# Kernel tuning notes

Hardware: AMD Instinct MI355X
Metric: run time of the kernel (lower is better)

## Reference

```python
import jax, jax.numpy as jnp
import numpy as np

COMMA_ID = 1010   # BERT wordpiece id for ','
H, NH, HD = 768, 8, 96
B, S = 64, 512
NSEG = 17         # 16 commas per row -> 17 segments
EPS = 1e-5


def setup_inputs() -> dict:
    key = jax.random.key(0)
    ks = jax.random.split(key, 16)
    text_hs = jax.random.normal(ks[0], (B, S, H), jnp.float32)
    cols_hs = jax.random.normal(ks[1], (B, S, H), jnp.float32)
    ids = jax.random.randint(ks[2], (B, S), 0, 30522)
    ids = jnp.where(ids == COMMA_ID, COMMA_ID + 1, ids)  # avoid accidental commas
    comma_pos = jnp.arange(16, 257, 16)                  # 16 commas per row
    ids = ids.at[:, comma_pos].set(COMMA_ID)
    sc = 0.02
    wq = jax.random.normal(ks[3], (H, H), jnp.float32) * sc
    wk = jax.random.normal(ks[4], (H, H), jnp.float32) * sc
    wv = jax.random.normal(ks[5], (H, H), jnp.float32) * sc
    bq = jnp.zeros((H,), jnp.float32)
    bk = jnp.zeros((H,), jnp.float32)
    bv = jnp.zeros((H,), jnp.float32)
    wo = jax.random.normal(ks[6], (H, H), jnp.float32) * sc
    bo = jnp.zeros((H,), jnp.float32)
    gamma = jnp.ones((H,), jnp.float32)
    beta = jnp.zeros((H,), jnp.float32)
    w_out = jax.random.normal(ks[7], (1, H), jnp.float32) * sc
    b_out = jnp.zeros((1,), jnp.float32)
    return dict(text_hs=text_hs, cols_hs=cols_hs, wq=wq, wk=wk, wv=wv,
                bq=bq, bk=bk, bv=bv, wo=wo, bo=bo, gamma=gamma, beta=beta,
                w_out=w_out, b_out=b_out, columns_input_ids=ids, n_segments=NSEG)


def _forward(text_hs, cols_hs, wq, wk, wv, bq, bk, bv, wo, bo,
             gamma, beta, w_out, b_out, columns_input_ids, n_segments):
    t = text_hs[:, 1:, :]   # drop first token, as in forward()  [B, L, H]
    c = cols_hs[:, 1:, :]
    L = t.shape[1]
    # --- nn.MultiheadAttention(query=cols, key=value=text), batch_first ---
    q = c @ wq.T + bq
    k = t @ wk.T + bk
    v = t @ wv.T + bv
    split = lambda x: x.reshape(x.shape[0], -1, NH, HD).transpose(0, 2, 1, 3)
    scores = jnp.einsum('bhqd,bhkd->bhqk', split(q), split(k)) / np.sqrt(HD).astype(np.float32)
    attn = jax.nn.softmax(scores, axis=-1)
    ctx = jnp.einsum('bhqk,bhkd->bhqd', attn, split(v))
    ctx = ctx.transpose(0, 2, 1, 3).reshape(c.shape[0], L, H)
    attn_out = ctx @ wo.T + bo
    # --- BatchNorm1d over channels (training-mode batch stats) ---
    xt = attn_out.transpose(0, 2, 1)            # [B, H, L]
    mu = xt.mean(axis=(0, 2), keepdims=True)
    var = xt.var(axis=(0, 2), keepdims=True)     # biased, as torch BN normalization
    xn = (xt - mu) / jnp.sqrt(var + EPS) * gamma[None, :, None] + beta[None, :, None]
    cross_out = c + xn.transpose(0, 2, 1)       # residual add
    fv = (cross_out @ w_out.T + b_out).squeeze(-1)   # [B, L] scores per token
    # --- compose_outputs: mean-pool comma-delimited ragged spans ---
    is_comma = columns_input_ids[:, :L] == COMMA_ID
    seg = jnp.cumsum(is_comma.astype(jnp.int32), axis=1) - is_comma.astype(jnp.int32)
    mask = (jnp.arange(L)[None, :] >= 1) & (~is_comma)    # slice_start=1, commas excluded
    oh = ((seg[:, :, None] == jnp.arange(n_segments)[None, None, :])
          & mask[:, :, None]).astype(fv.dtype)            # [B, L, J]
    sums = jnp.einsum('blj,bl->bj', oh, fv)
    cnt = oh.sum(axis=1)
    return sums / jnp.maximum(cnt, 1.0)                   # [B, n_segments]


def reference(text_hs, cols_hs, wq, wk, wv, bq, bk, bv, wo, bo,
              gamma, beta, w_out, b_out, columns_input_ids, n_segments):
    return _forward(text_hs, cols_hs, wq, wk, wv, bq, bk, bv, wo, bo,
                    gamma, beta, w_out, b_out, columns_input_ids, n_segments)
```

## Files before the change

### kernel.cpp

```cpp
#include <hip/hip_runtime.h>
#include <hip/hip_bf16.h>

#define COMMA_IDC 1010
#define NHEAD 8
#define Ll 511
#define Mrows 32704
#define NSEG 17

typedef __attribute__((ext_vector_type(8))) short bf16x8;
typedef __attribute__((ext_vector_type(4))) float f32x4;
typedef unsigned short u16;
typedef unsigned int u32;
typedef unsigned long long u64;

__device__ __forceinline__ u16 f2b(float f) {
  __hip_bfloat16 h = __float2bfloat16(f);
  return *reinterpret_cast<u16*>(&h);
}
__device__ __forceinline__ float b2f(u16 u) {
  u32 x = ((u32)u) << 16;
  return __builtin_bit_cast(float, x);
}

__device__ __forceinline__ void gld_lds16(const void* g, void* l) {
  __builtin_amdgcn_global_load_lds(
      (const __attribute__((address_space(1))) void*)(u64)g,
      (__attribute__((address_space(3))) void*)(u32)(u64)l,
      16, 0, 0);
}

#define MFMA16(a, b, c) __builtin_amdgcn_mfma_f32_16x16x32_bf16(a, b, c, 0, 0, 0)

__global__ void conv_sliced2(const float4* __restrict__ s0, const float4* __restrict__ s1,
                             ushort4* __restrict__ d0, ushort4* __restrict__ d1) {
  const float4* src = blockIdx.z ? s1 : s0;
  ushort4* dst = blockIdx.z ? d1 : d0;
  int b = blockIdx.y;
  int idx = blockIdx.x * 256 + threadIdx.x;
  if (idx >= Ll * 192) return;
  int l = idx / 192, c = idx - l * 192;
  float4 v = src[(b * 512 + l + 1) * 192 + c];
  ushort4 o; o.x = f2b(v.x); o.y = f2b(v.y); o.z = f2b(v.z); o.w = f2b(v.w);
  dst[(b * Ll + l) * 192 + c] = o;
}

__global__ void conv_w(const float4* __restrict__ wq, const float4* __restrict__ wk,
                       const float4* __restrict__ wv, const float4* __restrict__ wo,
                       ushort4* __restrict__ wqkvb, ushort4* __restrict__ wob) {
  int i = blockIdx.x * 256 + threadIdx.x;
  int seg = i / 147456, off = i - seg * 147456;
  const float4* s = (seg == 0) ? wq : ((seg == 1) ? wk : ((seg == 2) ? wv : wo));
  ushort4* d = (seg == 3) ? wob : (wqkvb + seg * 147456);
  float4 v = s[off];
  ushort4 o; o.x = f2b(v.x); o.y = f2b(v.y); o.z = f2b(v.z); o.w = f2b(v.w);
  d[off] = o;
}

__global__ void zero_kernel(float* p, int n) {
  int i = blockIdx.x * 256 + threadIdx.x;
  if (i < n) p[i] = 0.f;
}

#define LDA_(i, kk) (*(const bf16x8*)(sMem + bA + ((i) * 16 + fr) * 64 + ((((kk) * 4 + fq) ^ xm) << 3)))
#define LDW_(j, kk) (*(const bf16x8*)(sMem + bW + (((wc * 64 + (j) * 16) >> 7) * 8192) + \
                     (((wc * 64 + (j) * 16) & 127) + fr) * 64 + ((((kk) * 4 + fq) ^ xm) << 3)))
#define LGKM0 do { asm volatile("s_waitcnt lgkmcnt(0)" ::: "memory"); __builtin_amdgcn_sched_barrier(0); } while (0)

template<int NTILES, int NOUT, int QNT>
__global__ __launch_bounds__(512, 2) void gemm256(
    const u16* __restrict__ A0, const u16* __restrict__ A1, const u16* __restrict__ W,
    const float* __restrict__ b0, const float* __restrict__ b1, const float* __restrict__ b2,
    u16* __restrict__ outp)
{
  __shared__ __align__(16) u16 sMem[65536];
  const int tid = threadIdx.x;
  const int lane = tid & 63, wid = tid >> 6;
  const int fr = lane & 15, fq = lane >> 4;
  const int wr = wid >> 2, wc = wid & 3;
  const int xm = fr & 7;

  int fid = blockIdx.x;
  int xcd = fid & 7, w = fid >> 3;
  int mrow = xcd * 16 + w / NTILES;
  int ncol = w - (w / NTILES) * NTILES;
  const int m0 = mrow * 256, n0 = ncol * 256;
  const u16* __restrict__ A = (ncol < QNT) ? A0 : A1;

  const int rS = tid >> 3;
  const int cS = (tid & 7) ^ (rS & 7);
  const u16* gA0 = A + (u64)(m0 + rS) * 768 + cS * 8;
  const u16* gA1 = A + (u64)(m0 + 128 + rS) * 768 + cS * 8;
  const u16* gW0 = W + (u64)(n0 + rS) * 768 + cS * 8;
  const u16* gW1 = W + (u64)(n0 + 128 + rS) * 768 + cS * 8;
  const u32 st0 = tid * 8;

  f32x4 acc[8][4] = {};

  auto stage_all = [&](int buf, int kt) {
    const int kb = kt * 64;
    const u32 db = (u32)buf * 32768;
    gld_lds16(gA0 + kb, sMem + db + st0);
    gld_lds16(gA0 + kb + 49152, sMem + db + st0 + 4096);
    gld_lds16(gA1 + kb, sMem + db + 8192 + st0);
    gld_lds16(gA1 + kb + 49152, sMem + db + 8192 + st0 + 4096);
    gld_lds16(gW0 + kb, sMem + db + 16384 + st0);
    gld_lds16(gW0 + kb + 49152, sMem + db + 16384 + st0 + 4096);
    gld_lds16(gW1 + kb, sMem + db + 24576 + st0);
    gld_lds16(gW1 + kb + 49152, sMem + db + 24576 + st0 + 4096);
  };

  stage_all(0, 0);
  asm volatile("s_waitcnt vmcnt(0)" ::: "memory");
  __builtin_amdgcn_s_barrier();

  for (int kt = 0; kt < 12; ++kt) {
    const u32 db = (u32)(kt & 1) * 32768;
    const u32 bA = db + wr * 8192;
    const u32 bW = db + 16384;
    bf16x8 af[4][2], wf[2][2];

#pragma unroll
    for (int i = 0; i < 4; i++) { af[i][0] = LDA_(i, 0); af[i][1] = LDA_(i, 1); }
#pragma unroll
    for (int j = 0; j < 2; j++) { wf[j][0] = LDW_(j, 0); wf[j][1] = LDW_(j, 1); }
    __builtin_amdgcn_s_barrier();
    if (kt + 1 < 12) stage_all((kt + 1) & 1, kt + 1);
    LGKM0;
    __builtin_amdgcn_s_setprio(1);
#pragma unroll
    for (int i = 0; i < 4; i++)
#pragma unroll
      for (int j = 0; j < 2; j++) {
        acc[i][j] = MFMA16(af[i][0], wf[j][0], acc[i][j]);
        acc[i][j] = MFMA16(af[i][1], wf[j][1], acc[i][j]);
      }
    __builtin_amdgcn_s_setprio(0);
    __builtin_amdgcn_s_barrier();

#pragma unroll
    for (int j = 0; j < 2; j++) { wf[j][0] = LDW_(j + 2, 0); wf[j][1] = LDW_(j + 2, 1); }
    __builtin_amdgcn_s_barrier();
    LGKM0;
    __builtin_amdgcn_s_setprio(1);
#pragma unroll
    for (int i = 0; i < 4; i++)
#pragma unroll
      for (int j = 0; j < 2; j++) {
        acc[i][j + 2] = MFMA16(af[i][0], wf[j][0], acc[i][j + 2]);
        acc[i][j + 2] = MFMA16(af[i][1], wf[j][1], acc[i][j + 2]);
      }
    __builtin_amdgcn_s_setprio(0);
    __builtin_amdgcn_s_barrier();

#pragma unroll
    for (int i = 0; i < 4; i++) { af[i][0] = LDA_(i + 4, 0); af[i][1] = LDA_(i + 4, 1); }
#pragma unroll
    for (int j = 0; j < 2; j++) { wf[j][0] = LDW_(j, 0); wf[j][1] = LDW_(j, 1); }
    __builtin_amdgcn_s_barrier();
    LGKM0;
    __builtin_amdgcn_s_setprio(1);
#pragma unroll
    for (int i = 0; i < 4; i++)
#pragma unroll
      for (int j = 0; j < 2; j++) {
        acc[i + 4][j] = MFMA16(af[i][0], wf[j][0], acc[i + 4][j]);
        acc[i + 4][j] = MFMA16(af[i][1], wf[j][1], acc[i + 4][j]);
      }
    __builtin_amdgcn_s_setprio(0);
    __builtin_amdgcn_s_barrier();

#pragma unroll
    for (int j = 0; j < 2; j++) { wf[j][0] = LDW_(j + 2, 0); wf[j][1] = LDW_(j + 2, 1); }
    __builtin_amdgcn_s_barrier();
    LGKM0;
    __builtin_amdgcn_s_setprio(1);
#pragma unroll
    for (int i = 0; i < 4; i++)
#pragma unroll
      for (int j = 0; j < 2; j++) {
        acc[i + 4][j + 2] = MFMA16(af[i][0], wf[j][0], acc[i + 4][j + 2]);
        acc[i + 4][j + 2] = MFMA16(af[i][1], wf[j][1], acc[i + 4][j + 2]);
      }
    __builtin_amdgcn_s_setprio(0);
    asm volatile("s_waitcnt vmcnt(0)" ::: "memory");
    __builtin_amdgcn_s_barrier();
  }

  const float* bp = (n0 < 768) ? b0 : ((n0 < 1536) ? b1 : b2);
  const int bcol = n0 & 767;
  float bj[4];
#pragma unroll
  for (int j = 0; j < 4; j++) bj[j] = bp[bcol + wc * 64 + j * 16 + fr];

#pragma unroll
  for (int h = 0; h < 2; h++) {
    __syncthreads();
    if (wr == h) {
#pragma unroll
      for (int i = 0; i < 8; i++)
#pragma unroll
        for (int j = 0; j < 4; j++)
#pragma unroll
          for (int r = 0; r < 4; r++)
            sMem[(i * 16 + fq * 4 + r) * 264 + wc * 64 + j * 16 + fr] = f2b(acc[i][j][r] + bj[j]);
    }
    __syncthreads();
#pragma unroll
    for (int it = 0; it < 8; it++) {
      int chunk = tid + it * 512;
      int lr = chunk >> 5, ch = chunk & 31;
      *(bf16x8*)(outp + (u64)(m0 + h * 128 + lr) * NOUT + n0 + ch * 8) =
          *(const bf16x8*)(sMem + lr * 264 + ch * 8);
    }
  }
}

__global__ __launch_bounds__(256) void vtrans(const u16* __restrict__ QKV, u16* __restrict__ VT) {
  __shared__ __align__(16) u16 sT[128 * 128];
  int bh = blockIdx.y;
  int b = bh >> 3, h = bh & 7;
  int l0 = blockIdx.x * 128;
  u16* outp = VT + (u64)bh * 96 * 512;
  int t = threadIdx.x;
#pragma unroll
  for (int k = 0; k < 6; k++) {
    int c = t + k * 256;
    int l = c / 12, ch = c - l * 12;
    int lc = l0 + l; if (lc > 510) lc = 510;
    bf16x8 v = *(const bf16x8*)(QKV + (u64)(b * 511 + lc) * 2304 + 1536 + h * 96 + ch * 8);
    int chunk = l * 16 + (ch ^ ((l >> 3) & 7));
    *(bf16x8*)(sT + chunk * 8) = v;
  }
  __syncthreads();
#pragma unroll
  for (int k = 0; k < 6; k++) {
    int c = t + k * 256;
    int d = c >> 4, lch = c & 15;
    u16 vals[8];
#pragma unroll
    for (int k2 = 0; k2 < 8; k2++) {
      int r = lch * 8 + k2;
      int idx = r * 128 + (((d >> 3) ^ (lch & 7)) << 3) + (d & 7);
      vals[k2] = sT[idx];
    }
    bf16x8 o;
#pragma unroll
    for (int k2 = 0; k2 < 8; k2++) o[k2] = (short)vals[k2];
    *(bf16x8*)(outp + (u64)d * 512 + l0 + lch * 8) = o;
  }
}

#define PST 36
__global__ __launch_bounds__(256) void attn_kernel(
    const u16* __restrict__ QKV, const u16* __restrict__ VT, u16* __restrict__ ctxb)
{
  __shared__ __align__(16) u16 sK[32 * 96];
  __shared__ __align__(16) u16 sV[32 * 96];
  __shared__ __align__(16) u16 sP[4][16 * PST];
  const int tid = threadIdx.x, lane = tid & 63, wid = tid >> 6;
  int fid = blockIdx.x;
  int xcd = fid & 7, slot = (fid >> 3) & 3, grp = fid >> 5;
  int bh = grp * 8 + xcd;
  int b = bh >> 3, h = bh & 7;
  int q0 = slot * 128;
  const int fr = lane & 15, fq = lane >> 4;
  const u64 mb = (u64)(b * 511);
  const u64 hbV = (u64)bh * 96 * 512;

  bf16x8 qf[2][3];
#pragma unroll
  for (int sub = 0; sub < 2; sub++) {
    int qr = q0 + wid * 32 + sub * 16 + fr; if (qr > 510) qr = 510;
#pragma unroll
    for (int ks = 0; ks < 3; ks++)
      qf[sub][ks] = *(const bf16x8*)(QKV + (mb + qr) * 2304 + h * 96 + ks * 32 + fq * 8);
  }

  f32x4 ctx[2][6] = {};
  f32x4 sumP[2] = {};

  int cK1 = wid * 64 + lane;
  int kr1 = cK1 / 12, kc1 = cK1 - kr1 * 12;
  const u16* gK1 = QKV + (mb + kr1) * 2304 + 768 + h * 96 + kc1 * 8;
  int cK2 = 256 + cK1;
  int kr2 = cK2 / 12, kc2 = cK2 - kr2 * 12;
  const u16* gK2 = QKV + (mb + kr2) * 2304 + 768 + h * 96 + kc2 * 8;
  int cV1 = wid * 64 + lane;
  int dV1 = cV1 >> 2, jV1 = (cV1 & 3) ^ ((dV1 >> 1) & 3);
  const u16* gV1 = VT + hbV + (u64)dV1 * 512 + jV1 * 8;
  int cV2 = 256 + (wid - 2) * 64 + lane;
  int dV2 = cV2 >> 2, jV2 = (cV2 & 3) ^ ((dV2 >> 1) & 3);
  const u16* gV2 = VT + hbV + (u64)dV2 * 512 + jV2 * 8;

  u16* lK1 = sK + (u32)(wid * 64) * 8;
  u16* lK2 = sK + (u32)(256 + wid * 64) * 8;
  u16* lV1 = sV + (u32)(wid * 64) * 8;
  u16* lV2 = sV + (u32)(256 + (wid - 2) * 64) * 8;
  u16* pw = &sP[wid][0];

  const float cs = 0.10206207261596575f;
  const int cpx = fq ^ ((fr >> 1) & 3);

  for (int kv0 = 0; kv0 < 511; kv0 += 32) {
    __syncthreads();
    gld_lds16(gK1, lK1); gK1 += (u64)32 * 2304;
    if (wid < 2) { gld_lds16(gK2, lK2); gK2 += (u64)32 * 2304; }
    gld_lds16(gV1, lV1); gV1 += 32;
    if (wid >= 2) { gld_lds16(gV2, lV2); gV2 += 32; }
    __syncthreads();

    bf16x8 kf0[3], kf1[3];
#pragma unroll
    for (int ks = 0; ks < 3; ks++) {
      kf0[ks] = *(const bf16x8*)(sK + fr * 96 + ks * 32 + fq * 8);
      kf1[ks] = *(const bf16x8*)(sK + (16 + fr) * 96 + ks * 32 + fq * 8);
    }
    const bool ok1 = (kv0 + 16 + fr) < Ll;

#pragma unroll
    for (int sub = 0; sub < 2; sub++) {
      f32x4 s0 = {}, s1 = {};
#pragma unroll
      for (int ks = 0; ks < 3; ks++) {
        s0 = MFMA16(qf[sub][ks], kf0[ks], s0);
        s1 = MFMA16(qf[sub][ks], kf1[ks], s1);
      }
      float p0[4], p1[4];
#pragma unroll
      for (int r = 0; r < 4; r++) {
        p0[r] = __expf(s0[r] * cs);
        float e1 = __expf(s1[r] * cs);
        p1[r] = ok1 ? e1 : 0.f;
        sumP[sub][r] += p0[r] + p1[r];
      }
#pragma unroll
      for (int r = 0; r < 4; r++) {
        int row = fq * 4 + r;
        pw[row * PST + fr] = f2b(p0[r]);
        pw[row * PST + 16 + fr] = f2b(p1[r]);
      }
      bf16x8 pf = *(const bf16x8*)(pw + fr * PST + fq * 8);
#pragma unroll
      for (int df = 0; df < 6; df++) {
        bf16x8 vf = *(const bf16x8*)(sV + (df * 16 + fr) * 32 + cpx * 8);
        ctx[sub][df] = MFMA16(pf, vf, ctx[sub][df]);
      }
    }
  }

#pragma unroll
  for (int sub = 0; sub < 2; sub++) {
    float inv[4];
#pragma unroll
    for (int r = 0; r < 4; r++) {
      float s = sumP[sub][r];
      s += __shfl_xor(s, 1, 64);
      s += __shfl_xor(s, 2, 64);
      s += __shfl_xor(s, 4, 64);
      s += __shfl_xor(s, 8, 64);
      inv[r] = 1.f / s;
    }
#pragma unroll
    for (int df = 0; df < 6; df++) {
#pragma unroll
      for (int r = 0; r < 4; r++) {
        int q = q0 + wid * 32 + sub * 16 + fq * 4 + r;
        if (q < Ll)
          ctxb[(u64)(b * Ll + q) * 768 + h * 96 + df * 16 + fr] = f2b(ctx[sub][df][r] * inv[r]);
      }
    }
  }
}

__global__ __launch_bounds__(256) void stats_kernel(const u16* __restrict__ ao,
                                                    float* __restrict__ ssum, float* __restrict__ ssq)
{
  int t = threadIdx.x;
  int row0 = blockIdx.x * 128;
  int rowEnd = row0 + 128; if (rowEnd > Mrows) rowEnd = Mrows;
  float s[3] = {0.f, 0.f, 0.f}, q[3] = {0.f, 0.f, 0.f};
  for (int m = row0; m < rowEnd; m++) {
    const u16* rp = ao + (u64)m * 768;
#pragma unroll
    for (int i = 0; i < 3; i++) {
      float v = b2f(rp[t + i * 256]);
      s[i] += v; q[i] += v * v;
    }
  }
#pragma unroll
  for (int i = 0; i < 3; i++) {
    atomicAdd(&ssum[t + i * 256], s[i]);
    atomicAdd(&ssq[t + i * 256], q[i]);
  }
}

__global__ __launch_bounds__(256) void derived_kernel(
    const float* __restrict__ ssum, const float* __restrict__ ssq,
    const float* __restrict__ w_out, const float* __restrict__ b_out,
    const float* __restrict__ gamma, const float* __restrict__ beta,
    float* __restrict__ weff, float* __restrict__ consts)
{
  __shared__ float red[256];
  int t = threadIdx.x;
  float acc = 0.f;
  const float invN = 1.f / 32704.f;
#pragma unroll
  for (int i = 0; i < 3; i++) {
    int hh = t + i * 256;
    float mu = ssum[hh] * invN;
    float var = ssq[hh] * invN - mu * mu;
    float rstd = 1.f / sqrtf(var + 1e-5f);
    float we = w_out[hh] * gamma[hh] * rstd;
    weff[hh] = we;
    acc += w_out[hh] * beta[hh] - we * mu;
  }
  red[t] = acc; __syncthreads();
  for (int s = 128; s > 0; s >>= 1) { if (t < s) red[t] += red[t + s]; __syncthreads(); }
  if (t == 0) consts[0] = b_out[0] + red[0];
}

__global__ __launch_bounds__(256) void fv_kernel(
    const u16* __restrict__ ao, const u16* __restrict__ cb,
    const float* __restrict__ w_out, const float* __restrict__ weff,
    const float* __restrict__ consts, float* __restrict__ fv)
{
  int lane = threadIdx.x & 63, wid = threadIdx.x >> 6;
  int m = blockIdx.x * 4 + wid;
  if (m >= Mrows) return;
  const u16* ap = ao + (u64)m * 768;
  const u16* cp = cb + (u64)m * 768;
  float acc = 0.f;
#pragma unroll
  for (int i = 0; i < 12; i++) {
    int hh = lane + i * 64;
    acc += b2f(ap[hh]) * weff[hh] + b2f(cp[hh]) * w_out[hh];
  }
#pragma unroll
  for (int off = 1; off < 64; off <<= 1) acc += __shfl_xor(acc, off, 64);
  if (lane == 0) fv[m] = acc + consts[0];
}

__global__ __launch_bounds__(64) void seg_kernel(
    const float* __restrict__ fv, const int* __restrict__ ids, float* __restrict__ out)
{
  __shared__ float ssum[NSEG];
  __shared__ int scnt[NSEG];
  int lane = threadIdx.x;
  int b = blockIdx.x;
  if (lane < NSEG) { ssum[lane] = 0.f; scnt[lane] = 0; }
  __syncthreads();
  int carry = 0;
  for (int it = 0; it < 8; it++) {
    int l = it * 64 + lane;
    bool active = l < Ll;
    int id = active ? ids[b * 512 + l] : 0;
    bool comma = active && (id == COMMA_IDC);
    u64 cmask = __ballot(comma);
    int seg = carry + __popcll(cmask & ((1ull << lane) - 1ull));
    bool valid = active && (l >= 1) && !comma;
    if (valid && seg < NSEG) {
      atomicAdd(&ssum[seg], fv[b * Ll + l]);
      atomicAdd(&scnt[seg], 1);
    }
    carry += __popcll(cmask);
  }
  __syncthreads();
  if (lane < NSEG) {
    float c = (float)scnt[lane];
    out[b * NSEG + lane] = ssum[lane] / fmaxf(c, 1.f);
  }
}

extern "C" void kernel_launch(void* const* d_in, const int* in_sizes, int n_in,
                              void* d_out, int out_size, void* d_ws, size_t ws_size,
                              hipStream_t stream)
{
  const float* text  = (const float*)d_in[0];
  const float* cols  = (const float*)d_in[1];
  const float* wq    = (const float*)d_in[2];
  const float* wk    = (const float*)d_in[3];
  const float* wvp   = (const float*)d_in[4];
  const float* bq    = (const float*)d_in[5];
  const float* bk    = (const float*)d_in[6];
  const float* bv    = (const float*)d_in[7];
  const float* wo    = (const float*)d_in[8];
  const float* bo    = (const float*)d_in[9];
  const float* gamma = (const float*)d_in[10];
  const float* beta  = (const float*)d_in[11];
  const float* w_out = (const float*)d_in[12];
  const float* b_out = (const float*)d_in[13];
  const int*   ids   = (const int*)d_in[14];
  float* out = (float*)d_out;

  char* ws = (char*)d_ws;
  u16* cb    = (u16*)(ws + 0ull);
  u16* tb    = (u16*)(ws + 50331648ull);
  u16* wqkvb = (u16*)(ws + 100663296ull);
  u16* wob   = (u16*)(ws + 104202240ull);
  u16* QKVb  = (u16*)(ws + 105381888ull);
  u16* ctxb  = (u16*)(ws + 256376832ull);
  u16* VTb   = tb;
  u16* aob   = QKVb;
  float* ssum   = (float*)(ws + 105381888ull + 50331648ull);
  float* ssq    = ssum + 768;
  float* weff   = ssum + 1536;
  float* consts = ssum + 2304;
  float* fv     = (float*)((char*)ssum + 16384ull);

  conv_sliced2<<<dim3(384, 64, 2), 256, 0, stream>>>(
      (const float4*)cols, (const float4*)text, (ushort4*)cb, (ushort4*)tb);
  conv_w<<<2304, 256, 0, stream>>>(
      (const float4*)wq, (const float4*)wk, (const float4*)wvp, (const float4*)wo,
      (ushort4*)wqkvb, (ushort4*)wob);

  gemm256<9, 2304, 3><<<1152, 512, 0, stream>>>(cb, tb, wqkvb, bq, bk, bv, QKVb);
  vtrans<<<dim3(4, 512), 256, 0, stream>>>(QKVb, VTb);
  attn_kernel<<<2048, 256, 0, stream>>>(QKVb, VTb, ctxb);

  zero_kernel<<<6, 256, 0, stream>>>(ssum, 1536);
  gemm256<3, 768, 99><<<384, 512, 0, stream>>>(ctxb, ctxb, wob, bo, bo, bo, aob);
  stats_kernel<<<256, 256, 0, stream>>>(aob, ssum, ssq);
  derived_kernel<<<1, 256, 0, stream>>>(ssum, ssq, w_out, b_out, gamma, beta, weff, consts);
  fv_kernel<<<8176, 256, 0, stream>>>(aob, cb, w_out, weff, consts, fv);
  seg_kernel<<<64, 64, 0, stream>>>(fv, ids, out);
}
```

Before: 460.2 us.

## Fuse fp32 input conversion into QKV GEMM, BN stats into out-proj, widen attention tile

The separate fp32-to-bf16 slice/convert kernel is removed. The QKV GEMM now loads fp32 activations from the original tensors into registers, converts them, and writes them to LDS, double-buffered with a deeper prefetch. The output-projection GEMM accumulates BatchNorm column sums and sums of squares in its epilogue via atomics, which replaces the stats pass over the output. The attention kernel processes 64 keys per step instead of 32, with new LDS swizzles. The GEMM inner loop is also restructured to load all W fragments at once with fewer barriers, and fv reads the fp32 columns directly. This saves bandwidth and kernel launches, at the cost of register pressure, a different bf16 rounding path for the stats, and a more complex attention tile.

```diff
diff --git a/kernel.cpp b/kernel.cpp
--- a/kernel.cpp
+++ b/kernel.cpp
@@ -30,19 +30,7 @@
 }
 
 #define MFMA16(a, b, c) __builtin_amdgcn_mfma_f32_16x16x32_bf16(a, b, c, 0, 0, 0)
-
-__global__ void conv_sliced2(const float4* __restrict__ s0, const float4* __restrict__ s1,
-                             ushort4* __restrict__ d0, ushort4* __restrict__ d1) {
-  const float4* src = blockIdx.z ? s1 : s0;
-  ushort4* dst = blockIdx.z ? d1 : d0;
-  int b = blockIdx.y;
-  int idx = blockIdx.x * 256 + threadIdx.x;
-  if (idx >= Ll * 192) return;
-  int l = idx / 192, c = idx - l * 192;
-  float4 v = src[(b * 512 + l + 1) * 192 + c];
-  ushort4 o; o.x = f2b(v.x); o.y = f2b(v.y); o.z = f2b(v.z); o.w = f2b(v.w);
-  dst[(b * Ll + l) * 192 + c] = o;
-}
+#define LGKM0 do { asm volatile("s_waitcnt lgkmcnt(0)" ::: "memory"); __builtin_amdgcn_sched_barrier(0); } while (0)
 
 __global__ void conv_w(const float4* __restrict__ wq, const float4* __restrict__ wk,
                        const float4* __restrict__ wv, const float4* __restrict__ wo,
@@ -61,16 +49,15 @@
   if (i < n) p[i] = 0.f;
 }
 
-#define LDA_(i, kk) (*(const bf16x8*)(sMem + bA + ((i) * 16 + fr) * 64 + ((((kk) * 4 + fq) ^ xm) << 3)))
-#define LDW_(j, kk) (*(const bf16x8*)(sMem + bW + (((wc * 64 + (j) * 16) >> 7) * 8192) + \
+#define LDA(db, i, kk) (*(const bf16x8*)(sMem + (db) + wr * 8192 + ((i) * 16 + fr) * 64 + ((((kk) * 4 + fq) ^ xm) << 3)))
+#define LDW(db, j, kk) (*(const bf16x8*)(sMem + (db) + 16384 + (((wc * 64 + (j) * 16) >> 7) * 8192) + \
                      (((wc * 64 + (j) * 16) & 127) + fr) * 64 + ((((kk) * 4 + fq) ^ xm) << 3)))
-#define LGKM0 do { asm volatile("s_waitcnt lgkmcnt(0)" ::: "memory"); __builtin_amdgcn_sched_barrier(0); } while (0)
-
-template<int NTILES, int NOUT, int QNT>
+
+template<int NTILES, int NOUT, int QNT, bool AF32, bool DO_STATS>
 __global__ __launch_bounds__(512, 2) void gemm256(
-    const u16* __restrict__ A0, const u16* __restrict__ A1, const u16* __restrict__ W,
+    const void* __restrict__ A0v, const void* __restrict__ A1v, const u16* __restrict__ W,
     const float* __restrict__ b0, const float* __restrict__ b1, const float* __restrict__ b2,
-    u16* __restrict__ outp)
+    u16* __restrict__ outp, float* __restrict__ ssum, float* __restrict__ ssq)
 {
   __shared__ __align__(16) u16 sMem[65536];
   const int tid = threadIdx.x;
@@ -84,113 +71,167 @@
   int mrow = xcd * 16 + w / NTILES;
   int ncol = w - (w / NTILES) * NTILES;
   const int m0 = mrow * 256, n0 = ncol * 256;
-  const u16* __restrict__ A = (ncol < QNT) ? A0 : A1;
 
   const int rS = tid >> 3;
   const int cS = (tid & 7) ^ (rS & 7);
-  const u16* gA0 = A + (u64)(m0 + rS) * 768 + cS * 8;
-  const u16* gA1 = A + (u64)(m0 + 128 + rS) * 768 + cS * 8;
   const u16* gW0 = W + (u64)(n0 + rS) * 768 + cS * 8;
   const u16* gW1 = W + (u64)(n0 + 128 + rS) * 768 + cS * 8;
   const u32 st0 = tid * 8;
 
+  const float* fA = (ncol < QNT) ? (const float*)A0v : (const float*)A1v;
+  const u16*   uA = (ncol < QNT) ? (const u16*)A0v : (const u16*)A1v;
+  const float* aSrc[4];
+  u32 aDst[4];
+  if constexpr (AF32) {
+#pragma unroll
+    for (int c4 = 0; c4 < 4; c4++) {
+      int c = tid + c4 * 512;
+      int half = c >> 10, rowin = (c >> 3) & 127, p = c & 7;
+      int m = m0 + half * 128 + rowin;
+      if (m > Mrows - 1) m = Mrows - 1;
+      int srcrow = m + m / 511 + 1;
+      int s = p ^ (rowin & 7);
+      aSrc[c4] = fA + (u64)srcrow * 768 + s * 8;
+      aDst[c4] = (u32)(half * 8192 + rowin * 64 + p * 8);
+    }
+  }
+  const u16* gA0u = nullptr;
+  const u16* gA1u = nullptr;
+  if constexpr (!AF32) {
+    gA0u = uA + (u64)(m0 + rS) * 768 + cS * 8;
+    gA1u = uA + (u64)(m0 + 128 + rS) * 768 + cS * 8;
+  }
+
   f32x4 acc[8][4] = {};
-
-  auto stage_all = [&](int buf, int kt) {
+  bf16x8 af[4][2], wf[4][2];
+  float4 rA[8];
+
+  auto stageW = [&](int buf, int kt) {
+    const int kb = kt * 64;
+    const u32 db = (u32)buf * 32768 + 16384;
+    gld_lds16(gW0 + kb, sMem + db + st0);
+    gld_lds16(gW0 + kb + 49152, sMem + db + st0 + 4096);
+    gld_lds16(gW1 + kb, sMem + db + 8192 + st0);
+    gld_lds16(gW1 + kb + 49152, sMem + db + 8192 + st0 + 4096);
+  };
+  auto stageAu = [&](int buf, int kt) {
     const int kb = kt * 64;
     const u32 db = (u32)buf * 32768;
-    gld_lds16(gA0 + kb, sMem + db + st0);
-    gld_lds16(gA0 + kb + 49152, sMem + db + st0 + 4096);
-    gld_lds16(gA1 + kb, sMem + db + 8192 + st0);
-    gld_lds16(gA1 + kb + 49152, sMem + db + 8192 + st0 + 4096);
-    gld_lds16(gW0 + kb, sMem + db + 16384 + st0);
-    gld_lds16(gW0 + kb + 49152, sMem + db + 16384 + st0 + 4096);
-    gld_lds16(gW1 + kb, sMem + db + 24576 + st0);
-    gld_lds16(gW1 + kb + 49152, sMem + db + 24576 + st0 + 4096);
+    gld_lds16(gA0u + kb, sMem + db + st0);
+    gld_lds16(gA0u + kb + 49152, sMem + db + st0 + 4096);
+    gld_lds16(gA1u + kb, sMem + db + 8192 + st0);
+    gld_lds16(gA1u + kb + 49152, sMem + db + 8192 + st0 + 4096);
   };
-
-  stage_all(0, 0);
-  asm volatile("s_waitcnt vmcnt(0)" ::: "memory");
+  auto loadA = [&](int kt) {
+#pragma unroll
+    for (int c4 = 0; c4 < 4; c4++) {
+      rA[2 * c4]     = *(const float4*)(aSrc[c4] + kt * 64);
+      rA[2 * c4 + 1] = *(const float4*)(aSrc[c4] + kt * 64 + 4);
+    }
+  };
+  auto writeA = [&](int buf) {
+    const u32 db = (u32)buf * 32768;
+#pragma unroll
+    for (int c4 = 0; c4 < 4; c4++) {
+      const float4 x = rA[2 * c4], y = rA[2 * c4 + 1];
+      bf16x8 v;
+      v[0] = (short)f2b(x.x); v[1] = (short)f2b(x.y); v[2] = (short)f2b(x.z); v[3] = (short)f2b(x.w);
+      v[4] = (short)f2b(y.x); v[5] = (short)f2b(y.y); v[6] = (short)f2b(y.z); v[7] = (short)f2b(y.w);
+      *(bf16x8*)(sMem + db + aDst[c4]) = v;
+    }
+  };
+
+  if constexpr (AF32) {
+    stageW(0, 0);
+    loadA(0);
+    writeA(0);
+    loadA(1);
+  } else {
+    stageAu(0, 0);
+    stageW(0, 0);
+    asm volatile("s_waitcnt vmcnt(0)" ::: "memory");
+  }
+  LGKM0;
   __builtin_amdgcn_s_barrier();
 
   for (int kt = 0; kt < 12; ++kt) {
     const u32 db = (u32)(kt & 1) * 32768;
-    const u32 bA = db + wr * 8192;
-    const u32 bW = db + 16384;
-    bf16x8 af[4][2], wf[2][2];
-
-#pragma unroll
-    for (int i = 0; i < 4; i++) { af[i][0] = LDA_(i, 0); af[i][1] = LDA_(i, 1); }
-#pragma unroll
-    for (int j = 0; j < 2; j++) { wf[j][0] = LDW_(j, 0); wf[j][1] = LDW_(j, 1); }
-    __builtin_amdgcn_s_barrier();
-    if (kt + 1 < 12) stage_all((kt + 1) & 1, kt + 1);
-    LGKM0;
-    __builtin_amdgcn_s_setprio(1);
-#pragma unroll
-    for (int i = 0; i < 4; i++)
-#pragma unroll
-      for (int j = 0; j < 2; j++) {
-        acc[i][j] = MFMA16(af[i][0], wf[j][0], acc[i][j]);
-        acc[i][j] = MFMA16(af[i][1], wf[j][1], acc[i][j]);
-      }
-    __builtin_amdgcn_s_setprio(0);
-    __builtin_amdgcn_s_barrier();
-
-#pragma unroll
-    for (int j = 0; j < 2; j++) { wf[j][0] = LDW_(j + 2, 0); wf[j][1] = LDW_(j + 2, 1); }
+#pragma unroll
+    for (int i = 0; i < 4; i++) { af[i][0] = LDA(db, i, 0); af[i][1] = LDA(db, i, 1); }
+#pragma unroll
+    for (int j = 0; j < 4; j++) { wf[j][0] = LDW(db, j, 0); wf[j][1] = LDW(db, j, 1); }
+    if (kt + 1 < 12) {
+      if constexpr (AF32) {
+        writeA((kt + 1) & 1);
+        stageW((kt + 1) & 1, kt + 1);
+        if (kt + 2 < 12) loadA(kt + 2);
+      } else {
+        stageAu((kt + 1) & 1, kt + 1);
+        stageW((kt + 1) & 1, kt + 1);
+      }
+    }
     __builtin_amdgcn_s_barrier();
     LGKM0;
     __builtin_amdgcn_s_setprio(1);
 #pragma unroll
     for (int i = 0; i < 4; i++)
 #pragma unroll
-      for (int j = 0; j < 2; j++) {
-        acc[i][j + 2] = MFMA16(af[i][0], wf[j][0], acc[i][j + 2]);
-        acc[i][j + 2] = MFMA16(af[i][1], wf[j][1], acc[i][j + 2]);
+      for (int j = 0; j < 4; j++) {
+        acc[i][j] = MFMA16(af[i][0], wf[j][0], acc[i][j]);
+        acc[i][j] = MFMA16(af[i][1], wf[j][1], acc[i][j]);
       }
     __builtin_amdgcn_s_setprio(0);
     __builtin_amdgcn_s_barrier();
-
-#pragma unroll
-    for (int i = 0; i < 4; i++) { af[i][0] = LDA_(i + 4, 0); af[i][1] = LDA_(i + 4, 1); }
-#pragma unroll
-    for (int j = 0; j < 2; j++) { wf[j][0] = LDW_(j, 0); wf[j][1] = LDW_(j, 1); }
-    __builtin_amdgcn_s_barrier();
+#pragma unroll
+    for (int i = 0; i < 4; i++) { af[i][0] = LDA(db, i + 4, 0); af[i][1] = LDA(db, i + 4, 1); }
     LGKM0;
     __builtin_amdgcn_s_setprio(1);
 #pragma unroll
     for (int i = 0; i < 4; i++)
 #pragma unroll
-      for (int j = 0; j < 2; j++) {
+      for (int j = 0; j < 4; j++) {
         acc[i + 4][j] = MFMA16(af[i][0], wf[j][0], acc[i + 4][j]);
         acc[i + 4][j] = MFMA16(af[i][1], wf[j][1], acc[i + 4][j]);
       }
     __builtin_amdgcn_s_setprio(0);
+    if (kt + 1 < 12) {
+      if constexpr (AF32) {
+        if (kt + 2 < 12) { asm volatile("s_waitcnt vmcnt(8)" ::: "memory"); }
+        else             { asm volatile("s_waitcnt vmcnt(0)" ::: "memory"); }
+      } else {
+        asm volatile("s_waitcnt vmcnt(0)" ::: "memory");
+      }
+    }
     __builtin_amdgcn_s_barrier();
-
-#pragma unroll
-    for (int j = 0; j < 2; j++) { wf[j][0] = LDW_(j + 2, 0); wf[j][1] = LDW_(j + 2, 1); }
-    __builtin_amdgcn_s_barrier();
-    LGKM0;
-    __builtin_amdgcn_s_setprio(1);
-#pragma unroll
-    for (int i = 0; i < 4; i++)
-#pragma unroll
-      for (int j = 0; j < 2; j++) {
-        acc[i + 4][j + 2] = MFMA16(af[i][0], wf[j][0], acc[i + 4][j + 2]);
-        acc[i + 4][j + 2] = MFMA16(af[i][1], wf[j][1], acc[i + 4][j + 2]);
-      }
-    __builtin_amdgcn_s_setprio(0);
-    asm volatile("s_waitcnt vmcnt(0)" ::: "memory");
-    __builtin_amdgcn_s_barrier();
   }
 
   const float* bp = (n0 < 768) ? b0 : ((n0 < 1536) ? b1 : b2);
-  const int bcol = n0 & 767;
+  const int bcol = n0 % 768;
   float bj[4];
 #pragma unroll
   for (int j = 0; j < 4; j++) bj[j] = bp[bcol + wc * 64 + j * 16 + fr];
+
+  if constexpr (DO_STATS) {
+#pragma unroll
+    for (int j = 0; j < 4; j++) {
+      float s = 0.f, q = 0.f;
+#pragma unroll
+      for (int i = 0; i < 8; i++)
+#pragma unroll
+        for (int r = 0; r < 4; r++) {
+          int m = m0 + wr * 128 + i * 16 + fq * 4 + r;
+          float v = acc[i][j][r] + bj[j];
+          if (m < Mrows) { s += v; q += v * v; }
+        }
+      s += __shfl_xor(s, 16, 64); s += __shfl_xor(s, 32, 64);
+      q += __shfl_xor(q, 16, 64); q += __shfl_xor(q, 32, 64);
+      if (fq == 0) {
+        int col = n0 + wc * 64 + j * 16 + fr;
+        atomicAdd(&ssum[col], s);
+        atomicAdd(&ssq[col], q);
+      }
+    }
+  }
 
 #pragma unroll
   for (int h = 0; h < 2; h++) {
@@ -250,12 +291,12 @@
   }
 }
 
-#define PST 36
+#define PST 68
 __global__ __launch_bounds__(256) void attn_kernel(
     const u16* __restrict__ QKV, const u16* __restrict__ VT, u16* __restrict__ ctxb)
 {
-  __shared__ __align__(16) u16 sK[32 * 96];
-  __shared__ __align__(16) u16 sV[32 * 96];
+  __shared__ __align__(16) u16 sK[64 * 96];
+  __shared__ __align__(16) u16 sV[96 * 64];
   __shared__ __align__(16) u16 sP[4][16 * PST];
   const int tid = threadIdx.x, lane = tid & 63, wid = tid >> 6;
   int fid = blockIdx.x;
@@ -279,71 +320,79 @@
   f32x4 ctx[2][6] = {};
   f32x4 sumP[2] = {};
 
-  int cK1 = wid * 64 + lane;
-  int kr1 = cK1 / 12, kc1 = cK1 - kr1 * 12;
-  const u16* gK1 = QKV + (mb + kr1) * 2304 + 768 + h * 96 + kc1 * 8;
-  int cK2 = 256 + cK1;
-  int kr2 = cK2 / 12, kc2 = cK2 - kr2 * 12;
-  const u16* gK2 = QKV + (mb + kr2) * 2304 + 768 + h * 96 + kc2 * 8;
-  int cV1 = wid * 64 + lane;
-  int dV1 = cV1 >> 2, jV1 = (cV1 & 3) ^ ((dV1 >> 1) & 3);
-  const u16* gV1 = VT + hbV + (u64)dV1 * 512 + jV1 * 8;
-  int cV2 = 256 + (wid - 2) * 64 + lane;
-  int dV2 = cV2 >> 2, jV2 = (cV2 & 3) ^ ((dV2 >> 1) & 3);
-  const u16* gV2 = VT + hbV + (u64)dV2 * 512 + jV2 * 8;
-
-  u16* lK1 = sK + (u32)(wid * 64) * 8;
-  u16* lK2 = sK + (u32)(256 + wid * 64) * 8;
-  u16* lV1 = sV + (u32)(wid * 64) * 8;
-  u16* lV2 = sV + (u32)(256 + (wid - 2) * 64) * 8;
+  int kRow[3]; u32 kOffG[3], vOffG[3];
+  u16 *kDst[3], *vDst[3];
+#pragma unroll
+  for (int k = 0; k < 3; k++) {
+    int c = wid * 64 + lane + k * 256;
+    int r = c / 12, p = c - r * 12;
+    int s = p - (r % 12); if (s < 0) s += 12;
+    kRow[k] = r;
+    kOffG[k] = 768 + h * 96 + s * 8;
+    kDst[k] = sK + (u32)(wid * 64 + k * 256) * 8;
+    int d = c >> 3, pv = c & 7;
+    int sv = pv ^ (d & 7);
+    vOffG[k] = (u32)(d * 512 + sv * 8);
+    vDst[k] = sV + (u32)(wid * 64 + k * 256) * 8;
+  }
+
+  const float cs = 0.10206207261596575f;
   u16* pw = &sP[wid][0];
 
-  const float cs = 0.10206207261596575f;
-  const int cpx = fq ^ ((fr >> 1) & 3);
-
-  for (int kv0 = 0; kv0 < 511; kv0 += 32) {
+  for (int kv0 = 0; kv0 < 511; kv0 += 64) {
     __syncthreads();
-    gld_lds16(gK1, lK1); gK1 += (u64)32 * 2304;
-    if (wid < 2) { gld_lds16(gK2, lK2); gK2 += (u64)32 * 2304; }
-    gld_lds16(gV1, lV1); gV1 += 32;
-    if (wid >= 2) { gld_lds16(gV2, lV2); gV2 += 32; }
+#pragma unroll
+    for (int k = 0; k < 3; k++) {
+      int row = kv0 + kRow[k]; if (row > 510) row = 510;
+      gld_lds16(QKV + (mb + row) * 2304 + kOffG[k], kDst[k]);
+    }
+#pragma unroll
+    for (int k = 0; k < 3; k++)
+      gld_lds16(VT + hbV + vOffG[k] + kv0, vDst[k]);
     __syncthreads();
 
-    bf16x8 kf0[3], kf1[3];
-#pragma unroll
-    for (int ks = 0; ks < 3; ks++) {
-      kf0[ks] = *(const bf16x8*)(sK + fr * 96 + ks * 32 + fq * 8);
-      kf1[ks] = *(const bf16x8*)(sK + (16 + fr) * 96 + ks * 32 + fq * 8);
-    }
-    const bool ok1 = (kv0 + 16 + fr) < Ll;
+    bf16x8 kf[4][3];
+#pragma unroll
+    for (int kv16 = 0; kv16 < 4; kv16++) {
+      int r = kv16 * 16 + fr;
+      int rm = r % 12;
+#pragma unroll
+      for (int ks = 0; ks < 3; ks++) {
+        int sidx = ks * 4 + fq + rm; if (sidx >= 12) sidx -= 12;
+        kf[kv16][ks] = *(const bf16x8*)(sK + (r * 12 + sidx) * 8);
+      }
+    }
 
 #pragma unroll
     for (int sub = 0; sub < 2; sub++) {
-      f32x4 s0 = {}, s1 = {};
-#pragma unroll
-      for (int ks = 0; ks < 3; ks++) {
-        s0 = MFMA16(qf[sub][ks], kf0[ks], s0);
-        s1 = MFMA16(qf[sub][ks], kf1[ks], s1);
-      }
-      float p0[4], p1[4];
-#pragma unroll
-      for (int r = 0; r < 4; r++) {
-        p0[r] = __expf(s0[r] * cs);
-        float e1 = __expf(s1[r] * cs);
-        p1[r] = ok1 ? e1 : 0.f;
-        sumP[sub][r] += p0[r] + p1[r];
-      }
-#pragma unroll
-      for (int r = 0; r < 4; r++) {
-        int row = fq * 4 + r;
-        pw[row * PST + fr] = f2b(p0[r]);
-        pw[row * PST + 16 + fr] = f2b(p1[r]);
-      }
-      bf16x8 pf = *(const bf16x8*)(pw + fr * PST + fq * 8);
+      f32x4 s[4] = {};
+#pragma unroll
+      for (int kv16 = 0; kv16 < 4; kv16++)
+#pragma unroll
+        for (int ks = 0; ks < 3; ks++)
+          s[kv16] = MFMA16(qf[sub][ks], kf[kv16][ks], s[kv16]);
+
+#pragma unroll
+      for (int kv16 = 0; kv16 < 4; kv16++) {
+        bool ok = (kv0 + kv16 * 16 + fr) < Ll;
+#pragma unroll
+        for (int r = 0; r < 4; r++) {
+          float e = __expf(s[kv16][r] * cs);
+          e = ok ? e : 0.f;
+          sumP[sub][r] += e;
+          pw[(fq * 4 + r) * PST + kv16 * 16 + fr] = f2b(e);
+        }
+      }
+      bf16x8 pf0 = *(const bf16x8*)(pw + fr * PST + fq * 8);
+      bf16x8 pf1 = *(const bf16x8*)(pw + fr * PST + 32 + fq * 8);
 #pragma unroll
       for (int df = 0; df < 6; df++) {
-        bf16x8 vf = *(const bf16x8*)(sV + (df * 16 + fr) * 32 + cpx * 8);
-        ctx[sub][df] = MFMA16(pf, vf, ctx[sub][df]);
+        int row = df * 16 + fr;
+        int xv = fr & 7;
+        bf16x8 vf0 = *(const bf16x8*)(sV + row * 64 + ((fq ^ xv) << 3));
+        bf16x8 vf1 = *(const bf16x8*)(sV + row * 64 + (((4 + fq) ^ xv) << 3));
+        ctx[sub][df] = MFMA16(pf0, vf0, ctx[sub][df]);
+        ctx[sub][df] = MFMA16(pf1, vf1, ctx[sub][df]);
       }
     }
   }
@@ -369,28 +418,6 @@
           ctxb[(u64)(b * Ll + q) * 768 + h * 96 + df * 16 + fr] = f2b(ctx[sub][df][r] * inv[r]);
       }
     }
-  }
-}
-
-__global__ __launch_bounds__(256) void stats_kernel(const u16* __restrict__ ao,
-                                                    float* __restrict__ ssum, float* __restrict__ ssq)
-{
-  int t = threadIdx.x;
-  int row0 = blockIdx.x * 128;
-  int rowEnd = row0 + 128; if (rowEnd > Mrows) rowEnd = Mrows;
-  float s[3] = {0.f, 0.f, 0.f}, q[3] = {0.f, 0.f, 0.f};
-  for (int m = row0; m < rowEnd; m++) {
-    const u16* rp = ao + (u64)m * 768;
-#pragma unroll
-    for (int i = 0; i < 3; i++) {
-      float v = b2f(rp[t + i * 256]);
-      s[i] += v; q[i] += v * v;
-    }
-  }
-#pragma unroll
-  for (int i = 0; i < 3; i++) {
-    atomicAdd(&ssum[t + i * 256], s[i]);
-    atomicAdd(&ssq[t + i * 256], q[i]);
   }
 }
 
@@ -420,20 +447,21 @@
 }
 
 __global__ __launch_bounds__(256) void fv_kernel(
-    const u16* __restrict__ ao, const u16* __restrict__ cb,
+    const u16* __restrict__ ao, const float* __restrict__ cols,
     const float* __restrict__ w_out, const float* __restrict__ weff,
     const float* __restrict__ consts, float* __restrict__ fv)
 {
   int lane = threadIdx.x & 63, wid = threadIdx.x >> 6;
   int m = blockIdx.x * 4 + wid;
   if (m >= Mrows) return;
+  int bidx = m / 511, l = m - bidx * 511;
   const u16* ap = ao + (u64)m * 768;
-  const u16* cp = cb + (u64)m * 768;
+  const float* cp = cols + (u64)(bidx * 512 + l + 1) * 768;
   float acc = 0.f;
 #pragma unroll
   for (int i = 0; i < 12; i++) {
     int hh = lane + i * 64;
-    acc += b2f(ap[hh]) * weff[hh] + b2f(cp[hh]) * w_out[hh];
+    acc += b2f(ap[hh]) * weff[hh] + cp[hh] * w_out[hh];
   }
 #pragma unroll
   for (int off = 1; off < 64; off <<= 1) acc += __shfl_xor(acc, off, 64);
@@ -493,34 +521,31 @@
   float* out = (float*)d_out;
 
   char* ws = (char*)d_ws;
-  u16* cb    = (u16*)(ws + 0ull);
-  u16* tb    = (u16*)(ws + 50331648ull);
-  u16* wqkvb = (u16*)(ws + 100663296ull);
-  u16* wob   = (u16*)(ws + 104202240ull);
-  u16* QKVb  = (u16*)(ws + 105381888ull);
-  u16* ctxb  = (u16*)(ws + 256376832ull);
-  u16* VTb   = tb;
-  u16* aob   = QKVb;
-  float* ssum   = (float*)(ws + 105381888ull + 50331648ull);
+  u16* VTb   = (u16*)(ws + 0ull);
+  u16* wqkvb = (u16*)(ws + 50331648ull);
+  u16* wob   = (u16*)(ws + 53870592ull);
+  float* ssum   = (float*)(ws + 55050240ull);
   float* ssq    = ssum + 768;
   float* weff   = ssum + 1536;
   float* consts = ssum + 2304;
-  float* fv     = (float*)((char*)ssum + 16384ull);
-
-  conv_sliced2<<<dim3(384, 64, 2), 256, 0, stream>>>(
-      (const float4*)cols, (const float4*)text, (ushort4*)cb, (ushort4*)tb);
+  float* fv     = (float*)(ws + 55050240ull + 16384ull);
+  u16* QKVb  = (u16*)(ws + 56623104ull);
+  u16* ctxb  = (u16*)(ws + 207618048ull);
+  u16* aob   = QKVb;
+
   conv_w<<<2304, 256, 0, stream>>>(
       (const float4*)wq, (const float4*)wk, (const float4*)wvp, (const float4*)wo,
       (ushort4*)wqkvb, (ushort4*)wob);
-
-  gemm256<9, 2304, 3><<<1152, 512, 0, stream>>>(cb, tb, wqkvb, bq, bk, bv, QKVb);
+  zero_kernel<<<6, 256, 0, stream>>>(ssum, 1536);
+
+  gemm256<9, 2304, 3, true, false><<<1152, 512, 0, stream>>>(
+      cols, text, wqkvb, bq, bk, bv, QKVb, nullptr, nullptr);
   vtrans<<<dim3(4, 512), 256, 0, stream>>>(QKVb, VTb);
   attn_kernel<<<2048, 256, 0, stream>>>(QKVb, VTb, ctxb);
 
-  zero_kernel<<<6, 256, 0, stream>>>(ssum, 1536);
-  gemm256<3, 768, 99><<<384, 512, 0, stream>>>(ctxb, ctxb, wob, bo, bo, bo, aob);
-  stats_kernel<<<256, 256, 0, stream>>>(aob, ssum, ssq);
+  gemm256<3, 768, 99, false, true><<<384, 512, 0, stream>>>(
+      ctxb, ctxb, wob, bo, bo, bo, aob, ssum, ssq);
   derived_kernel<<<1, 256, 0, stream>>>(ssum, ssq, w_out, b_out, gamma, beta, weff, consts);
-  fv_kernel<<<8176, 256, 0, stream>>>(aob, cb, w_out, weff, consts, fv);
+  fv_kernel<<<8176, 256, 0, stream>>>(aob, cols, w_out, weff, consts, fv);
   seg_kernel<<<64, 64, 0, stream>>>(fv, ids, out);
 }
```

After: 462.5 us. Within noise of the previous version (+0.5%).
